# Kernel tuning notes

Hardware: AMD Instinct MI355X
Metric: run time of the kernel (lower is better)

Reference implementation:

```python
import jax, jax.numpy as jnp
import numpy as np
from jax import lax

MAX_C = 16       # MAX_MERGE_NUMS
COND_THRES = 0.2
IOU_THRES = 0.3
CLASS_OFFSET = 1e4  # shift per-class so cross-class BEV IoU == 0 (emulates per-class loop)


def setup_inputs() -> dict:
    key = jax.random.key(0)
    k1, k2, k3, k4, k5 = jax.random.split(key, 5)
    B, N = 4, 4096
    # realistic 3D boxes: centers, positive sizes, heading
    centers = jax.random.normal(k1, (B, N, 3), jnp.float32) * 20.0
    sizes = jax.random.uniform(k2, (B, N, 3), jnp.float32, 0.5, 4.5)
    heading = jax.random.uniform(k3, (B, N, 1), jnp.float32, -np.pi, np.pi)
    boxes = jnp.concatenate([centers, sizes, heading], -1)  # [B,N,7]
    scores = jax.random.uniform(k4, (B, N), jnp.float32)
    labels = jax.random.randint(k5, (B, N), 0, 3, jnp.int32)
    kw = jax.random.split(jax.random.fold_in(key, 1), 2)
    W1 = jax.random.normal(kw[0], (7, 64), jnp.float32) * 0.3
    b1 = jnp.zeros((64,), jnp.float32)
    W2 = jax.random.normal(kw[1], (64, 1), jnp.float32) * 0.3
    b2 = jnp.zeros((1,), jnp.float32)
    return {"boxes": boxes, "scores": scores, "labels": labels,
            "W1": W1, "b1": b1, "W2": W2, "b2": b2}


def _nms_merge_frame(boxes, scores, labels, W1, b1, W2, b2):
    # boxes [N,7], scores [N], labels [N] int32
    N = boxes.shape[0]
    valid = scores > COND_THRES                       # cond_mask
    skey = jnp.where(valid, scores, -jnp.inf)
    order = jnp.argsort(-skey)                        # score descending
    boxes, scores = boxes[order], scores[order]
    labels, valid = labels[order], valid[order]

    # nearest-BEV (axis-aligned) IoU; class offset keeps classes disjoint
    off = labels.astype(boxes.dtype) * CLASS_OFFSET
    cx, cy = boxes[:, 0] + off, boxes[:, 1]
    hx, hy = boxes[:, 3] * 0.5, boxes[:, 4] * 0.5
    x1, x2, y1, y2 = cx - hx, cx + hx, cy - hy, cy + hy
    ix = jnp.clip(jnp.minimum(x2[:, None], x2[None]) - jnp.maximum(x1[:, None], x1[None]), 0.0)
    iy = jnp.clip(jnp.minimum(y2[:, None], y2[None]) - jnp.maximum(y1[:, None], y1[None]), 0.0)
    inter = ix * iy                                   # [N,N]
    area = (x2 - x1) * (y2 - y1)
    iou = inter / jnp.clip(area[:, None] + area[None] - inter, 1e-6)
    overlap = iou > IOU_THRES                         # includes self

    # greedy clustering: highest-score remaining box leads its cluster
    def body(i, st):
        alive, cid = st
        lead = alive[i]
        take = alive & overlap[i] & lead
        cid = jnp.where(take, i, cid)
        return alive & (~take), cid
    alive, cid = lax.fori_loop(0, N, body,
                               (valid, jnp.full((N,), -1, jnp.int32)))
    leader = cid == jnp.arange(N, dtype=jnp.int32)    # cluster representatives

    # rank of each box within its cluster (score order preserved)
    idx = jnp.arange(N)
    same = (cid[None, :] == cid[:, None]) & (cid[:, None] >= 0)
    rank = (same & (idx[None, :] < idx[:, None])).sum(-1)  # [N]

    # scatter up to MAX_C members per cluster (zero-padded buffers)
    dest = jnp.where((cid >= 0) & (rank < MAX_C), cid, N)  # N = dump row
    clusters = jnp.zeros((N + 1, MAX_C, 7), boxes.dtype)
    clusters = clusters.at[dest, jnp.minimum(rank, MAX_C - 1)].set(boxes)[:N]

    # merge network: per-box MLP -> softmax weights over cluster slots
    h = jax.nn.relu(clusters @ W1 + b1)               # [N,MAX_C,64]
    logits = (h @ W2 + b2)[..., 0]                    # [N,MAX_C]
    slot_ok = jnp.any(clusters != 0, -1)
    logits = jnp.where(slot_ok, logits, -1e9)
    w = jax.nn.softmax(logits, -1)
    merged = jnp.einsum('nc,ncd->nd', w, clusters)    # [N,7]

    # masked scatter: non-positive merged sizes fall back to leader sizes
    size = jnp.where(merged[:, 3:6] <= 0, boxes[:, 3:6], merged[:, 3:6])
    out_box = jnp.concatenate([merged[:, :3], size, merged[:, 6:7]], -1)
    info = jnp.concatenate([out_box, scores[:, None],
                            labels.astype(boxes.dtype)[:, None]], -1)  # [N,9]
    info = jnp.where(leader[:, None], info, 0.0)
    return info, leader


def reference(boxes, scores, labels, W1, b1, W2, b2):
    info, leader = jax.vmap(_nms_merge_frame,
                            in_axes=(0, 0, 0, None, None, None, None))(
        boxes, scores, labels, W1, b1, W2, b2)
    return info, leader
```

## Files before the change

kernel.cpp:

```cpp
#include <hip/hip_runtime.h>
#include <stdint.h>

#pragma clang fp contract(off)

#define BF 4
#define NN 4096
#define MAXC 16
#define PL 2048
#define WL 32
#define WF 24
#define TRI_CAP (64 * (WL * (WL + 1) / 2))

typedef unsigned long long u64;
typedef uint32_t u32;

#define WAVE_SYNC() asm volatile("s_waitcnt lgkmcnt(0)" ::: "memory")

__device__ __forceinline__ u64 shfl64(u64 v, int src) {
  return (u64)__shfl((long long)v, src, 64);
}
__device__ __forceinline__ u64 readlane64(u64 v, int l) {
  u32 lo = (u32)__builtin_amdgcn_readlane((int)(u32)v, l);
  u32 hi = (u32)__builtin_amdgcn_readlane((int)(u32)(v >> 32), l);
  return ((u64)hi << 32) | lo;
}
__device__ __forceinline__ u64 greedy64_iso(u64 D, u64 rem, u64 onlyme) {
  u64 lead = 0;
  while (rem) {
    u64 t = D & rem;
    u64 iso = __ballot(t == onlyme) & rem;
    lead |= iso;
    rem &= ~iso;
    if (!rem) break;
    int b = __builtin_ctzll(rem);
    lead |= 1ull << b;
    rem &= ~readlane64(D, b);
    if (!rem) break;
    b = __builtin_ctzll(rem);
    lead |= 1ull << b;
    rem &= ~readlane64(D, b);
  }
  return lead;
}

__global__ __launch_bounds__(256) void rg_kernel(
    const float* __restrict__ scores, const float* __restrict__ boxes,
    const int* __restrict__ labels,
    float* __restrict__ sboxes, float* __restrict__ sscore, float* __restrict__ slabel,
    int* __restrict__ lab_slot, int* __restrict__ loc_slot,
    int* __restrict__ pglob,
    float* __restrict__ px1, float* __restrict__ px2, float* __restrict__ py1,
    float* __restrict__ py2, float* __restrict__ parea,
    int* __restrict__ VbufL)
{
  __shared__ u64 keys[NN];
  __shared__ int cnt[4][64];
  __shared__ int lcnt[4][64];
  __shared__ int vc[4][3];
  const int f = blockIdx.x >> 6, rb = blockIdx.x & 63;
  const int tid = threadIdx.x, wave = tid >> 6, lane = tid & 63;
  for (int s = 0; s < 16; s++) {
    int idx = tid + 256 * s;
    float sc = scores[f * NN + idx];
    bool valid = sc > 0.2f;
    int lab = labels[f * NN + idx];
    u32 bits = __float_as_uint(sc);
    u32 m = bits ^ ((bits >> 31) ? 0xFFFFFFFFu : 0x80000000u);
    u32 hi = valid ? ~m : 0xFFFFFFFFu;
    u32 lo = ((u32)idx << 2) | (valid ? (u32)lab : 3u);
    keys[idx] = ((u64)hi << 32) | lo;
  }
  __syncthreads();
  if (rb == 0) {
    int c0 = 0, c1 = 0, c2 = 0;
    const int base = wave * 1024;
    for (int s = 0; s < 16; s++) {
      u32 lb = (u32)keys[base + s * 64 + lane] & 3u;
      c0 += (lb == 0); c1 += (lb == 1); c2 += (lb == 2);
    }
    for (int off = 32; off; off >>= 1) {
      c0 += __shfl_xor(c0, off, 64);
      c1 += __shfl_xor(c1, off, 64);
      c2 += __shfl_xor(c2, off, 64);
    }
    if (lane == 0) { vc[wave][0] = c0; vc[wave][1] = c1; vc[wave][2] = c2; }
  }
  const int row = rb * 64 + lane;
  const u64 mykey = keys[row];
  const u32 mylab = (u32)mykey & 3u;
  int c = 0, lc = 0;
  const int j0 = wave * 1024;
#pragma unroll 8
  for (int j = j0; j < j0 + 1024; j++) {
    u64 kj = keys[j];
    bool lt = kj < mykey;
    c += lt ? 1 : 0;
    lc += (lt && (((u32)kj & 3u) == mylab)) ? 1 : 0;
  }
  cnt[wave][lane] = c;
  lcnt[wave][lane] = lc;
  __syncthreads();
  if (rb == 0 && wave == 1 && lane < 3)
    VbufL[f * 3 + lane] = vc[0][lane] + vc[1][lane] + vc[2][lane] + vc[3][lane];
  if (wave == 0) {
    int rank = cnt[0][lane] + cnt[1][lane] + cnt[2][lane] + cnt[3][lane];
    int loc  = lcnt[0][lane] + lcnt[1][lane] + lcnt[2][lane] + lcnt[3][lane];
    const int i = row;
    const float* bp = boxes + (size_t)(f * NN + i) * 7;
    float b0 = bp[0], b1v = bp[1], b2v = bp[2], b3 = bp[3], b4 = bp[4], b5 = bp[5], b6 = bp[6];
    int lab = labels[f * NN + i];
    float sc = scores[f * NN + i];
    const int o = f * NN + rank;
    float* sb = sboxes + (size_t)o * 7;
    sb[0] = b0; sb[1] = b1v; sb[2] = b2v; sb[3] = b3; sb[4] = b4; sb[5] = b5; sb[6] = b6;
    sscore[o] = sc;
    slabel[o] = (float)lab;
    if (mylab < 3u) {
      int pi = (f * 3 + (int)mylab) * PL + loc;
      float off = (float)mylab * 10000.0f;
      float cx = b0 + off, cy = b1v;
      float hx = b3 * 0.5f, hy = b4 * 0.5f;
      float x1 = cx - hx, x2 = cx + hx, y1 = cy - hy, y2 = cy + hy;
      float area = (x2 - x1) * (y2 - y1);
      pglob[pi] = rank;
      px1[pi] = x1; px2[pi] = x2; py1[pi] = y1; py2[pi] = y2; parea[pi] = area;
      lab_slot[o] = (int)mylab; loc_slot[o] = loc;
    } else {
      lab_slot[o] = -1; loc_slot[o] = -1;
    }
  }
}

__global__ __launch_bounds__(256) void mask_kernel(
    const float* __restrict__ px1, const float* __restrict__ px2,
    const float* __restrict__ py1, const float* __restrict__ py2,
    const float* __restrict__ parea, const int* __restrict__ pglob,
    const int* __restrict__ VbufL,
    u64* __restrict__ maskP, u64* __restrict__ triT)
{
  __shared__ float4 cbox[1024];
  __shared__ float carea[1024];
  const int bx = blockIdx.x;
  const int fl = bx >> 8, rem = bx & 255;
  const int rt = rem >> 1, wt = rem & 1;
  const int r0 = rt * 16;
  const int Vl = VbufL[fl];
  if (r0 >= Vl) return;
  if (wt * 1024 >= Vl) return;
  const int tid = threadIdx.x;
  const int ncol = Vl - wt * 1024;
  const int nload = (ncol < 1024) ? ncol : 1024;
  for (int q = tid; q < nload; q += 256) {
    int c = fl * PL + wt * 1024 + q;
    cbox[q] = make_float4(px1[c], px2[c], py1[c], py2[c]);
    carea[q] = parea[c];
  }
  __syncthreads();
  const int row = r0 + (tid & 15);
  const int wl = tid >> 4;
  const int cw = wt * 16 + wl;
  const int nc = Vl - cw * 64;
  if (row >= Vl || nc <= 0) return;
  const int rg = fl * PL + row;
  const float rx1 = px1[rg], rx2 = px2[rg], ry1 = py1[rg], ry2 = py2[rg], ra = parea[rg];
  u64 bits = 0;
  const int qb = wl * 64;
  for (int b = 0; b < 64; b++) {
    float4 cb = cbox[qb + b];
    float ca = carea[qb + b];
    float ix = fminf(rx2, cb.y) - fmaxf(rx1, cb.x);
    ix = fmaxf(ix, 0.0f);
    float iy = fminf(ry2, cb.w) - fmaxf(ry1, cb.z);
    iy = fmaxf(iy, 0.0f);
    float inter = ix * iy;
    float den = fmaxf((ra + ca) - inter, 1e-6f);
    float iou = inter / den;
    bits |= ((u64)(iou > 0.3f)) << b;
  }
  if (nc < 64) bits &= (1ull << nc) - 1ull;
  const int f = fl / 3;
  const int p = pglob[fl * PL + row];
  maskP[((size_t)f * NN + p) * WL + cw] = bits;
  if (row >= 64 * cw) {
    const int W = (Vl + 63) >> 6;
    int base = 64 * (cw * W - (cw * (cw - 1)) / 2);
    triT[(size_t)fl * TRI_CAP + base + (row - 64 * cw)] = bits;
  }
}

__global__ __launch_bounds__(64) void nms_kernel(
    const u64* __restrict__ triT, const int* __restrict__ VbufL,
    u64* __restrict__ leadersP)
{
  __shared__ u64 tri[64 * (WF * (WF + 1) / 2) + 128];
  const int fl = blockIdx.x, lane = threadIdx.x;
  const int Vl = VbufL[fl];
  const int W = (Vl + 63) >> 6;
  const u64* mT = triT + (size_t)fl * TRI_CAP;
  const u64 onlyme = 1ull << lane;
  u64 alive = 0;
  if (lane < WL) {
    int rb = Vl - 64 * lane;
    alive = (rb >= 64) ? ~0ull : ((rb > 0) ? ((1ull << rb) - 1ull) : 0ull);
  }
  u64 myLead = 0;

  if (W > 0 && W <= WF) {
    const int totw = 64 * (W * (W + 1) / 2);
    const int nch = (totw * 8 + 1023) >> 10;
    const char* g = (const char*)mT;
    char* l = (char*)tri;
    int batch = 0;
    for (int it = 0; it < nch; it++) {
      __builtin_amdgcn_global_load_lds(
          (const __attribute__((address_space(1))) unsigned int*)(g + (size_t)it * 1024 + (size_t)lane * 16),
          (__attribute__((address_space(3))) unsigned int*)(l + (size_t)it * 1024),
          16, 0, 0);
      if (++batch == 48) {
        asm volatile("s_waitcnt vmcnt(0)" ::: "memory");
        batch = 0;
      }
    }
    asm volatile("s_waitcnt vmcnt(0)" ::: "memory");
    int offw = 0;
    u64 D = tri[lane];
    for (int w = 0; w < W; w++) {
      const int offw_next = offw + 64 * (W - w);
      u64 Dnext = (w + 1 < W) ? tri[offw_next + lane] : 0;
      u64 lead = greedy64_iso(D, readlane64(alive, w), onlyme);
      if (lane == w) myLead = lead;
      if (lead) {
        const u64* strm = tri + offw;
        int v = w + 1;
        for (; v + 3 < W; v += 4) {
          u64 a0 = strm[64 * (v - w) + lane];
          u64 a1 = strm[64 * (v + 1 - w) + lane];
          u64 a2 = strm[64 * (v + 2 - w) + lane];
          u64 a3 = strm[64 * (v + 3 - w) + lane];
          u64 c0 = __ballot((a0 & lead) != 0ull);
          u64 c1 = __ballot((a1 & lead) != 0ull);
          u64 c2 = __ballot((a2 & lead) != 0ull);
          u64 c3 = __ballot((a3 & lead) != 0ull);
          if (lane == v)     alive &= ~c0;
          if (lane == v + 1) alive &= ~c1;
          if (lane == v + 2) alive &= ~c2;
          if (lane == v + 3) alive &= ~c3;
        }
        for (; v < W; v++) {
          u64 a0 = strm[64 * (v - w) + lane];
          u64 c0 = __ballot((a0 & lead) != 0ull);
          if (lane == v) alive &= ~c0;
        }
      }
      D = Dnext;
      offw = offw_next;
    }
  } else if (W > 0) {
    int offw = 0;
    for (int w = 0; w < W; w++) {
      const u64* strm = mT + offw;
      u64 D = strm[lane];
      u64 lead = greedy64_iso(D, readlane64(alive, w), onlyme);
      if (lane == w) myLead = lead;
      if (lead) {
        for (int v = w + 1; v < W; v++) {
          u64 a0 = strm[64 * (v - w) + lane];
          u64 c0 = __ballot((a0 & lead) != 0ull);
          if (lane == v) alive &= ~c0;
        }
      }
      offw += 64 * (W - w);
    }
  }
  if (lane < WL) leadersP[fl * WL + lane] = myLead;
}

__global__ __launch_bounds__(256) void cid_kernel(
    const u64* __restrict__ maskP, const u64* __restrict__ leadersP,
    const int* __restrict__ lab_slot, const int* __restrict__ loc_slot,
    const int* __restrict__ VbufL, int* __restrict__ cidP)
{
  const int g = blockIdx.x * 4 + (threadIdx.x >> 6);
  const int lane = threadIdx.x & 63;
  const int f = g >> 12, p = g & (NN - 1);
  const int l = lab_slot[f * NN + p];
  if (l < 0) return;
  const int fl = f * 3 + l;
  const int loc = loc_slot[f * NN + p];
  const int Wl = (VbufL[fl] + 63) >> 6;
  u64 L = 0, m = 0;
  if (lane < Wl) {
    L = leadersP[fl * WL + lane];
    m = maskP[((size_t)f * NN + p) * WL + lane];
  }
  const int g6 = loc >> 6, b6 = loc & 63;
  u64 pmask = (lane < g6) ? ~0ull
            : (lane == g6 ? ((b6 == 63) ? ~0ull : ((1ull << (b6 + 1)) - 1ull)) : 0ull);
  u64 v = m & L & pmask;
  u64 bl = __ballot(v != 0ull);
  int cid = -1;
  if (bl != 0ull) {
    int w = __builtin_ctzll(bl);
    u64 vw = shfl64(v, w);
    cid = w * 64 + __builtin_ctzll(vw);
  }
  if (lane == 0) cidP[fl * PL + loc] = cid;
}

__global__ __launch_bounds__(256) void mm_kernel(
    const u64* __restrict__ maskP, const u64* __restrict__ leadersP,
    const int* __restrict__ cidP, const int* __restrict__ lab_slot,
    const int* __restrict__ loc_slot, const int* __restrict__ pglob,
    const int* __restrict__ VbufL,
    const float* __restrict__ sboxes, const float* __restrict__ sscore,
    const float* __restrict__ slabel,
    const float* __restrict__ W1, const float* __restrict__ b1,
    const float* __restrict__ W2, const float* __restrict__ b2,
    float* __restrict__ out)
{
  __shared__ int   mlistS[4][MAXC];
  __shared__ float mbS[4][MAXC][7];
  __shared__ float lgS[4][MAXC];
  __shared__ float wnS[4][MAXC];
  const int wv = threadIdx.x >> 6, lane = threadIdx.x & 63;
  const int bi = blockIdx.x * 4 + wv;
  const int f = bi >> 12, i = bi & (NN - 1);
  const int o = f * NN + i;
  float* info = out + (size_t)o * 9;
  float* lead = out + (size_t)BF * NN * 9 + o;
  const int l = lab_slot[o];
  bool isLead = false;
  int loc = 0, fl = 0;
  if (l >= 0) {
    fl = f * 3 + l;
    loc = loc_slot[o];
    isLead = (leadersP[fl * WL + (loc >> 6)] >> (loc & 63)) & 1ull;
  }
  if (!isLead) {
    if (lane < 9) info[lane] = 0.0f;
    if (lane == 0) *lead = 0.0f;
    return;
  }
  int* mlist = mlistS[wv];
  float (*mb)[7] = mbS[wv];
  float* lg = lgS[wv];
  float* wn = wnS[wv];
  const u64* mrow = maskP + (size_t)o * WL;
  const int Wl = (VbufL[fl] + 63) >> 6;
  int total = 0;
  for (int w = loc >> 6; w < Wl && total < MAXC; w++) {
    u64 word = mrow[w];
    int pos = w * 64 + lane;
    bool cand = ((word >> lane) & 1ull) && (cidP[fl * PL + pos] == loc);
    u64 mbal = __ballot(cand);
    int r = __popcll(mbal & ((1ull << lane) - 1ull));
    int slot = total + r;
    if (cand && slot < MAXC) mlist[slot] = pglob[fl * PL + pos];
    total += __popcll(mbal);
  }
  const int cnt = min(total, MAXC);
  WAVE_SYNC();
  if (lane < cnt) {
    int j = mlist[lane];
    const float* bp = sboxes + (size_t)(f * NN + j) * 7;
    for (int d = 0; d < 7; d++) mb[lane][d] = bp[d];
  }
  float w1r[7];
  for (int d = 0; d < 7; d++) w1r[d] = W1[d * 64 + lane];
  const float b1c = b1[lane], w2c = W2[lane], b2v = b2[0];
  WAVE_SYNC();
  for (int s = 0; s < cnt; s++) {
    float t = b1c;
    for (int d = 0; d < 7; d++) t += mb[s][d] * w1r[d];
    float h = fmaxf(t, 0.0f);
    float v = h * w2c;
    for (int off2 = 32; off2 > 0; off2 >>= 1) v += __shfl_xor(v, off2, 64);
    if (lane == 0) lg[s] = v + b2v;
  }
  WAVE_SYNC();
  float mx = -1e30f;
  for (int s = 0; s < cnt; s++) mx = fmaxf(mx, lg[s]);
  float den = 0.0f;
  for (int s = 0; s < cnt; s++) den += expf(lg[s] - mx);
  if (lane < cnt) wn[lane] = expf(lg[lane] - mx) / den;
  WAVE_SYNC();
  float val = 0.0f;
  if (lane < 7) {
    float acc = 0.0f;
    for (int s = 0; s < cnt; s++) acc += wn[s] * mb[s][lane];
    val = acc;
    if (lane >= 3 && lane <= 5 && val <= 0.0f) val = sboxes[(size_t)o * 7 + lane];
  } else if (lane == 7) {
    val = sscore[o];
  } else if (lane == 8) {
    val = slabel[o];
  }
  if (lane < 9) info[lane] = val;
  if (lane == 0) *lead = 1.0f;
}

extern "C" void kernel_launch(void* const* d_in, const int* in_sizes, int n_in,
                              void* d_out, int out_size, void* d_ws, size_t ws_size,
                              hipStream_t stream)
{
  const float* boxes  = (const float*)d_in[0];
  const float* scores = (const float*)d_in[1];
  const int*   labels = (const int*)d_in[2];
  const float* W1     = (const float*)d_in[3];
  const float* b1     = (const float*)d_in[4];
  const float* W2     = (const float*)d_in[5];
  const float* b2     = (const float*)d_in[6];
  float* out = (float*)d_out;

  char* ws = (char*)d_ws;
  size_t off = 0;
  auto alloc = [&](size_t bytes) -> void* {
    void* p = ws + off;
    off = (off + bytes + 255) & ~(size_t)255;
    return p;
  };
  float* sboxes  = (float*)alloc((size_t)BF * NN * 7 * 4);
  float* sscore  = (float*)alloc((size_t)BF * NN * 4);
  float* slabel  = (float*)alloc((size_t)BF * NN * 4);
  int*   lab_slot= (int*)  alloc((size_t)BF * NN * 4);
  int*   loc_slot= (int*)  alloc((size_t)BF * NN * 4);
  int*   pglob   = (int*)  alloc((size_t)BF * 3 * PL * 4);
  float* px1     = (float*)alloc((size_t)BF * 3 * PL * 4);
  float* px2     = (float*)alloc((size_t)BF * 3 * PL * 4);
  float* py1     = (float*)alloc((size_t)BF * 3 * PL * 4);
  float* py2     = (float*)alloc((size_t)BF * 3 * PL * 4);
  float* parea   = (float*)alloc((size_t)BF * 3 * PL * 4);
  int*   VbufL   = (int*)  alloc((size_t)BF * 3 * 4);
  u64*   leadersP= (u64*)  alloc((size_t)BF * 3 * WL * 8);
  int*   cidP    = (int*)  alloc((size_t)BF * 3 * PL * 4);
  u64*   maskP   = (u64*)  alloc((size_t)BF * NN * WL * 8);
  u64*   triT    = (u64*)  alloc((size_t)BF * 3 * TRI_CAP * 8);
  (void)  alloc(32768);

  rg_kernel<<<BF * 64, 256, 0, stream>>>(scores, boxes, labels, sboxes,
                                         sscore, slabel, lab_slot, loc_slot,
                                         pglob, px1, px2, py1, py2, parea,
                                         VbufL);
  mask_kernel<<<BF * 3 * 256, 256, 0, stream>>>(px1, px2, py1, py2, parea,
                                                pglob, VbufL, maskP, triT);
  nms_kernel<<<BF * 3, 64, 0, stream>>>(triT, VbufL, leadersP);
  cid_kernel<<<BF * NN / 4, 256, 0, stream>>>(maskP, leadersP, lab_slot,
                                              loc_slot, VbufL, cidP);
  mm_kernel<<<BF * NN / 4, 256, 0, stream>>>(maskP, leadersP, cidP, lab_slot,
                                             loc_slot, pglob, VbufL, sboxes,
                                             sscore, slabel, W1, b1, W2, b2, out);
}
```

Baseline: 156.8 us.

## Fuse five pipeline kernels into one persistent kernel with grid barriers

Replaces the five separate launches (rank/gather, IoU mask, NMS, cluster-id, merge) with a single persistent kernel of 256 blocks. Stages are separated by atomic-counter grid barriers, and a memset resets the counters before each launch. The aim is to remove per-launch overhead and inter-kernel gaps. In exchange, the mask, cid and merge stages run with a fixed 256-block grid in grid-stride loops, and NMS still runs on only 12 single-wave blocks while the rest of the grid waits at a barrier. The spin barriers rely on all blocks being co-resident and have a timeout escape.

New measurement: 438.6 us. 180% more time.

```diff
diff --git a/kernel.cpp b/kernel.cpp
--- a/kernel.cpp
+++ b/kernel.cpp
@@ -42,376 +42,378 @@
   }
   return lead;
 }
-
-__global__ __launch_bounds__(256) void rg_kernel(
-    const float* __restrict__ scores, const float* __restrict__ boxes,
-    const int* __restrict__ labels,
-    float* __restrict__ sboxes, float* __restrict__ sscore, float* __restrict__ slabel,
-    int* __restrict__ lab_slot, int* __restrict__ loc_slot,
-    int* __restrict__ pglob,
-    float* __restrict__ px1, float* __restrict__ px2, float* __restrict__ py1,
-    float* __restrict__ py2, float* __restrict__ parea,
-    int* __restrict__ VbufL)
+__device__ __forceinline__ int loadVl(const int* VbufL, int fl) {
+  int v = VbufL[fl];
+  return (v < 0) ? 0 : ((v > PL) ? PL : v);
+}
+
+__device__ __forceinline__ void gbar(int* bar, int k) {
+  __syncthreads();
+  __threadfence();
+  if (threadIdx.x == 0) {
+    atomicAdd(&bar[k], 1);
+    long long t0 = clock64();
+    while (__hip_atomic_load(&bar[k], __ATOMIC_RELAXED,
+                             __HIP_MEMORY_SCOPE_AGENT) < (int)gridDim.x) {
+      __builtin_amdgcn_s_sleep(2);
+      if (clock64() - t0 > (3LL << 30)) break;
+    }
+  }
+  __syncthreads();
+  __threadfence();
+}
+
+struct Prm {
+  const float* scores; const float* boxes; const int* labels;
+  const float* W1; const float* b1; const float* W2; const float* b2;
+  float* sboxes; float* sscore; float* slabel;
+  int* lab_slot; int* loc_slot; int* pglob;
+  float* px1; float* px2; float* py1; float* py2; float* parea;
+  int* VbufL; u64* leadersP; int* cidP; u64* maskP; u64* triT;
+  int* bar;
+  float* out;
+};
+
+__global__ __launch_bounds__(256, 1) void fused_kernel(Prm pr)
 {
-  __shared__ u64 keys[NN];
-  __shared__ int cnt[4][64];
-  __shared__ int lcnt[4][64];
-  __shared__ int vc[4][3];
-  const int f = blockIdx.x >> 6, rb = blockIdx.x & 63;
+  __shared__ u64 SM[19500];
   const int tid = threadIdx.x, wave = tid >> 6, lane = tid & 63;
-  for (int s = 0; s < 16; s++) {
-    int idx = tid + 256 * s;
-    float sc = scores[f * NN + idx];
-    bool valid = sc > 0.2f;
-    int lab = labels[f * NN + idx];
-    u32 bits = __float_as_uint(sc);
-    u32 m = bits ^ ((bits >> 31) ? 0xFFFFFFFFu : 0x80000000u);
-    u32 hi = valid ? ~m : 0xFFFFFFFFu;
-    u32 lo = ((u32)idx << 2) | (valid ? (u32)lab : 3u);
-    keys[idx] = ((u64)hi << 32) | lo;
-  }
-  __syncthreads();
-  if (rb == 0) {
-    int c0 = 0, c1 = 0, c2 = 0;
-    const int base = wave * 1024;
+  const u64 ltmask = (1ull << lane) - 1ull;
+
+  {
+    u64* keys = SM;
+    int* cnt  = (int*)&SM[4096];
+    int* lcnt = (int*)&SM[4224];
+    int* vc   = (int*)&SM[4352];
+    const int f = blockIdx.x >> 6, rb = blockIdx.x & 63;
     for (int s = 0; s < 16; s++) {
-      u32 lb = (u32)keys[base + s * 64 + lane] & 3u;
-      c0 += (lb == 0); c1 += (lb == 1); c2 += (lb == 2);
-    }
-    for (int off = 32; off; off >>= 1) {
-      c0 += __shfl_xor(c0, off, 64);
-      c1 += __shfl_xor(c1, off, 64);
-      c2 += __shfl_xor(c2, off, 64);
-    }
-    if (lane == 0) { vc[wave][0] = c0; vc[wave][1] = c1; vc[wave][2] = c2; }
-  }
-  const int row = rb * 64 + lane;
-  const u64 mykey = keys[row];
-  const u32 mylab = (u32)mykey & 3u;
-  int c = 0, lc = 0;
-  const int j0 = wave * 1024;
+      int idx = tid + 256 * s;
+      float sc = pr.scores[f * NN + idx];
+      bool valid = sc > 0.2f;
+      int lab = pr.labels[f * NN + idx];
+      u32 bits = __float_as_uint(sc);
+      u32 m = bits ^ ((bits >> 31) ? 0xFFFFFFFFu : 0x80000000u);
+      u32 hi = valid ? ~m : 0xFFFFFFFFu;
+      u32 lo = ((u32)idx << 2) | (valid ? (u32)lab : 3u);
+      keys[idx] = ((u64)hi << 32) | lo;
+    }
+    __syncthreads();
+    if (rb == 0) {
+      int c0 = 0, c1 = 0, c2 = 0;
+      const int base = wave * 1024;
+      for (int s = 0; s < 16; s++) {
+        u32 lb = (u32)keys[base + s * 64 + lane] & 3u;
+        c0 += (lb == 0); c1 += (lb == 1); c2 += (lb == 2);
+      }
+      for (int off = 32; off; off >>= 1) {
+        c0 += __shfl_xor(c0, off, 64);
+        c1 += __shfl_xor(c1, off, 64);
+        c2 += __shfl_xor(c2, off, 64);
+      }
+      if (lane == 0) { vc[wave * 3 + 0] = c0; vc[wave * 3 + 1] = c1; vc[wave * 3 + 2] = c2; }
+    }
+    const int row = rb * 64 + lane;
+    const u64 mykey = keys[row];
+    const u32 mylab = (u32)mykey & 3u;
+    int c = 0, lc = 0;
+    const int j0 = wave * 1024;
 #pragma unroll 8
-  for (int j = j0; j < j0 + 1024; j++) {
-    u64 kj = keys[j];
-    bool lt = kj < mykey;
-    c += lt ? 1 : 0;
-    lc += (lt && (((u32)kj & 3u) == mylab)) ? 1 : 0;
-  }
-  cnt[wave][lane] = c;
-  lcnt[wave][lane] = lc;
-  __syncthreads();
-  if (rb == 0 && wave == 1 && lane < 3)
-    VbufL[f * 3 + lane] = vc[0][lane] + vc[1][lane] + vc[2][lane] + vc[3][lane];
-  if (wave == 0) {
-    int rank = cnt[0][lane] + cnt[1][lane] + cnt[2][lane] + cnt[3][lane];
-    int loc  = lcnt[0][lane] + lcnt[1][lane] + lcnt[2][lane] + lcnt[3][lane];
-    const int i = row;
-    const float* bp = boxes + (size_t)(f * NN + i) * 7;
-    float b0 = bp[0], b1v = bp[1], b2v = bp[2], b3 = bp[3], b4 = bp[4], b5 = bp[5], b6 = bp[6];
-    int lab = labels[f * NN + i];
-    float sc = scores[f * NN + i];
-    const int o = f * NN + rank;
-    float* sb = sboxes + (size_t)o * 7;
-    sb[0] = b0; sb[1] = b1v; sb[2] = b2v; sb[3] = b3; sb[4] = b4; sb[5] = b5; sb[6] = b6;
-    sscore[o] = sc;
-    slabel[o] = (float)lab;
-    if (mylab < 3u) {
-      int pi = (f * 3 + (int)mylab) * PL + loc;
-      float off = (float)mylab * 10000.0f;
-      float cx = b0 + off, cy = b1v;
-      float hx = b3 * 0.5f, hy = b4 * 0.5f;
-      float x1 = cx - hx, x2 = cx + hx, y1 = cy - hy, y2 = cy + hy;
-      float area = (x2 - x1) * (y2 - y1);
-      pglob[pi] = rank;
-      px1[pi] = x1; px2[pi] = x2; py1[pi] = y1; py2[pi] = y2; parea[pi] = area;
-      lab_slot[o] = (int)mylab; loc_slot[o] = loc;
-    } else {
-      lab_slot[o] = -1; loc_slot[o] = -1;
-    }
-  }
-}
-
-__global__ __launch_bounds__(256) void mask_kernel(
-    const float* __restrict__ px1, const float* __restrict__ px2,
-    const float* __restrict__ py1, const float* __restrict__ py2,
-    const float* __restrict__ parea, const int* __restrict__ pglob,
-    const int* __restrict__ VbufL,
-    u64* __restrict__ maskP, u64* __restrict__ triT)
-{
-  __shared__ float4 cbox[1024];
-  __shared__ float carea[1024];
-  const int bx = blockIdx.x;
-  const int fl = bx >> 8, rem = bx & 255;
-  const int rt = rem >> 1, wt = rem & 1;
-  const int r0 = rt * 16;
-  const int Vl = VbufL[fl];
-  if (r0 >= Vl) return;
-  if (wt * 1024 >= Vl) return;
-  const int tid = threadIdx.x;
-  const int ncol = Vl - wt * 1024;
-  const int nload = (ncol < 1024) ? ncol : 1024;
-  for (int q = tid; q < nload; q += 256) {
-    int c = fl * PL + wt * 1024 + q;
-    cbox[q] = make_float4(px1[c], px2[c], py1[c], py2[c]);
-    carea[q] = parea[c];
-  }
-  __syncthreads();
-  const int row = r0 + (tid & 15);
-  const int wl = tid >> 4;
-  const int cw = wt * 16 + wl;
-  const int nc = Vl - cw * 64;
-  if (row >= Vl || nc <= 0) return;
-  const int rg = fl * PL + row;
-  const float rx1 = px1[rg], rx2 = px2[rg], ry1 = py1[rg], ry2 = py2[rg], ra = parea[rg];
-  u64 bits = 0;
-  const int qb = wl * 64;
-  for (int b = 0; b < 64; b++) {
-    float4 cb = cbox[qb + b];
-    float ca = carea[qb + b];
-    float ix = fminf(rx2, cb.y) - fmaxf(rx1, cb.x);
-    ix = fmaxf(ix, 0.0f);
-    float iy = fminf(ry2, cb.w) - fmaxf(ry1, cb.z);
-    iy = fmaxf(iy, 0.0f);
-    float inter = ix * iy;
-    float den = fmaxf((ra + ca) - inter, 1e-6f);
-    float iou = inter / den;
-    bits |= ((u64)(iou > 0.3f)) << b;
-  }
-  if (nc < 64) bits &= (1ull << nc) - 1ull;
-  const int f = fl / 3;
-  const int p = pglob[fl * PL + row];
-  maskP[((size_t)f * NN + p) * WL + cw] = bits;
-  if (row >= 64 * cw) {
+    for (int j = j0; j < j0 + 1024; j++) {
+      u64 kj = keys[j];
+      bool lt = kj < mykey;
+      c += lt ? 1 : 0;
+      lc += (lt && (((u32)kj & 3u) == mylab)) ? 1 : 0;
+    }
+    cnt[wave * 64 + lane] = c;
+    lcnt[wave * 64 + lane] = lc;
+    __syncthreads();
+    if (rb == 0 && wave == 1 && lane < 3)
+      pr.VbufL[f * 3 + lane] = vc[0 * 3 + lane] + vc[1 * 3 + lane]
+                             + vc[2 * 3 + lane] + vc[3 * 3 + lane];
+    if (wave == 0) {
+      int rank = cnt[lane] + cnt[64 + lane] + cnt[128 + lane] + cnt[192 + lane];
+      int loc  = lcnt[lane] + lcnt[64 + lane] + lcnt[128 + lane] + lcnt[192 + lane];
+      const int i = row;
+      const float* bp = pr.boxes + (size_t)(f * NN + i) * 7;
+      float b0 = bp[0], b1v = bp[1], b2v = bp[2], b3 = bp[3], b4 = bp[4], b5 = bp[5], b6 = bp[6];
+      int lab = pr.labels[f * NN + i];
+      float sc = pr.scores[f * NN + i];
+      const int o = f * NN + rank;
+      float* sb = pr.sboxes + (size_t)o * 7;
+      sb[0] = b0; sb[1] = b1v; sb[2] = b2v; sb[3] = b3; sb[4] = b4; sb[5] = b5; sb[6] = b6;
+      pr.sscore[o] = sc;
+      pr.slabel[o] = (float)lab;
+      if (mylab < 3u) {
+        int pi = (f * 3 + (int)mylab) * PL + loc;
+        float off = (float)mylab * 10000.0f;
+        float cx = b0 + off, cy = b1v;
+        float hx = b3 * 0.5f, hy = b4 * 0.5f;
+        float x1 = cx - hx, x2 = cx + hx, y1 = cy - hy, y2 = cy + hy;
+        float area = (x2 - x1) * (y2 - y1);
+        pr.pglob[pi] = rank;
+        pr.px1[pi] = x1; pr.px2[pi] = x2; pr.py1[pi] = y1; pr.py2[pi] = y2;
+        pr.parea[pi] = area;
+        pr.lab_slot[o] = (int)mylab; pr.loc_slot[o] = loc;
+      } else {
+        pr.lab_slot[o] = -1; pr.loc_slot[o] = -1;
+      }
+    }
+  }
+  gbar(pr.bar, 0);
+
+  {
+    float4* cbox = (float4*)SM;
+    float*  carea = (float*)&SM[2048];
+    for (int vt = blockIdx.x; vt < BF * 3 * 256; vt += 256) {
+      __syncthreads();
+      const int fl = vt >> 8, rem = vt & 255;
+      const int rt = rem >> 1, wt = rem & 1;
+      const int r0 = rt * 16;
+      const int Vl = loadVl(pr.VbufL, fl);
+      const bool act = (r0 < Vl) && (wt * 1024 < Vl);
+      if (act) {
+        const int ncol = Vl - wt * 1024;
+        const int nload = (ncol < 1024) ? ncol : 1024;
+        for (int q = tid; q < nload; q += 256) {
+          int cc = fl * PL + wt * 1024 + q;
+          cbox[q] = make_float4(pr.px1[cc], pr.px2[cc], pr.py1[cc], pr.py2[cc]);
+          carea[q] = pr.parea[cc];
+        }
+      }
+      __syncthreads();
+      if (!act) continue;
+      const int row = r0 + (tid & 15);
+      const int wl = tid >> 4;
+      const int cw = wt * 16 + wl;
+      const int nc = Vl - cw * 64;
+      if (row < Vl && nc > 0) {
+        const int rg = fl * PL + row;
+        const float rx1 = pr.px1[rg], rx2 = pr.px2[rg];
+        const float ry1 = pr.py1[rg], ry2 = pr.py2[rg], ra = pr.parea[rg];
+        u64 bits = 0;
+        const int qb = wl * 64;
+        for (int b = 0; b < 64; b++) {
+          float4 cb = cbox[qb + b];
+          float ca = carea[qb + b];
+          float ix = fminf(rx2, cb.y) - fmaxf(rx1, cb.x);
+          ix = fmaxf(ix, 0.0f);
+          float iy = fminf(ry2, cb.w) - fmaxf(ry1, cb.z);
+          iy = fmaxf(iy, 0.0f);
+          float inter = ix * iy;
+          float den = fmaxf((ra + ca) - inter, 1e-6f);
+          float iou = inter / den;
+          bits |= ((u64)(iou > 0.3f)) << b;
+        }
+        if (nc < 64) bits &= (1ull << nc) - 1ull;
+        const int f = fl / 3;
+        const int p = pr.pglob[fl * PL + row] & (NN - 1);
+        pr.maskP[((size_t)f * NN + p) * WL + cw] = bits;
+        if (row >= 64 * cw) {
+          const int W = (Vl + 63) >> 6;
+          int base = 64 * (cw * W - (cw * (cw - 1)) / 2);
+          pr.triT[(size_t)fl * TRI_CAP + base + (row - 64 * cw)] = bits;
+        }
+      }
+    }
+  }
+  gbar(pr.bar, 1);
+
+  if (blockIdx.x < BF * 3 && wave == 0) {
+    u64* tri = SM;
+    const int fl = blockIdx.x;
+    const int Vl = loadVl(pr.VbufL, fl);
     const int W = (Vl + 63) >> 6;
-    int base = 64 * (cw * W - (cw * (cw - 1)) / 2);
-    triT[(size_t)fl * TRI_CAP + base + (row - 64 * cw)] = bits;
-  }
-}
-
-__global__ __launch_bounds__(64) void nms_kernel(
-    const u64* __restrict__ triT, const int* __restrict__ VbufL,
-    u64* __restrict__ leadersP)
-{
-  __shared__ u64 tri[64 * (WF * (WF + 1) / 2) + 128];
-  const int fl = blockIdx.x, lane = threadIdx.x;
-  const int Vl = VbufL[fl];
-  const int W = (Vl + 63) >> 6;
-  const u64* mT = triT + (size_t)fl * TRI_CAP;
-  const u64 onlyme = 1ull << lane;
-  u64 alive = 0;
-  if (lane < WL) {
-    int rb = Vl - 64 * lane;
-    alive = (rb >= 64) ? ~0ull : ((rb > 0) ? ((1ull << rb) - 1ull) : 0ull);
-  }
-  u64 myLead = 0;
-
-  if (W > 0 && W <= WF) {
-    const int totw = 64 * (W * (W + 1) / 2);
-    const int nch = (totw * 8 + 1023) >> 10;
-    const char* g = (const char*)mT;
-    char* l = (char*)tri;
-    int batch = 0;
-    for (int it = 0; it < nch; it++) {
-      __builtin_amdgcn_global_load_lds(
-          (const __attribute__((address_space(1))) unsigned int*)(g + (size_t)it * 1024 + (size_t)lane * 16),
-          (__attribute__((address_space(3))) unsigned int*)(l + (size_t)it * 1024),
-          16, 0, 0);
-      if (++batch == 48) {
-        asm volatile("s_waitcnt vmcnt(0)" ::: "memory");
-        batch = 0;
-      }
-    }
-    asm volatile("s_waitcnt vmcnt(0)" ::: "memory");
-    int offw = 0;
-    u64 D = tri[lane];
-    for (int w = 0; w < W; w++) {
-      const int offw_next = offw + 64 * (W - w);
-      u64 Dnext = (w + 1 < W) ? tri[offw_next + lane] : 0;
-      u64 lead = greedy64_iso(D, readlane64(alive, w), onlyme);
-      if (lane == w) myLead = lead;
-      if (lead) {
-        const u64* strm = tri + offw;
-        int v = w + 1;
-        for (; v + 3 < W; v += 4) {
-          u64 a0 = strm[64 * (v - w) + lane];
-          u64 a1 = strm[64 * (v + 1 - w) + lane];
-          u64 a2 = strm[64 * (v + 2 - w) + lane];
-          u64 a3 = strm[64 * (v + 3 - w) + lane];
-          u64 c0 = __ballot((a0 & lead) != 0ull);
-          u64 c1 = __ballot((a1 & lead) != 0ull);
-          u64 c2 = __ballot((a2 & lead) != 0ull);
-          u64 c3 = __ballot((a3 & lead) != 0ull);
-          if (lane == v)     alive &= ~c0;
-          if (lane == v + 1) alive &= ~c1;
-          if (lane == v + 2) alive &= ~c2;
-          if (lane == v + 3) alive &= ~c3;
-        }
-        for (; v < W; v++) {
-          u64 a0 = strm[64 * (v - w) + lane];
-          u64 c0 = __ballot((a0 & lead) != 0ull);
-          if (lane == v) alive &= ~c0;
-        }
-      }
-      D = Dnext;
-      offw = offw_next;
-    }
-  } else if (W > 0) {
-    int offw = 0;
-    for (int w = 0; w < W; w++) {
-      const u64* strm = mT + offw;
-      u64 D = strm[lane];
-      u64 lead = greedy64_iso(D, readlane64(alive, w), onlyme);
-      if (lane == w) myLead = lead;
-      if (lead) {
-        for (int v = w + 1; v < W; v++) {
-          u64 a0 = strm[64 * (v - w) + lane];
-          u64 c0 = __ballot((a0 & lead) != 0ull);
-          if (lane == v) alive &= ~c0;
-        }
-      }
-      offw += 64 * (W - w);
-    }
-  }
-  if (lane < WL) leadersP[fl * WL + lane] = myLead;
-}
-
-__global__ __launch_bounds__(256) void cid_kernel(
-    const u64* __restrict__ maskP, const u64* __restrict__ leadersP,
-    const int* __restrict__ lab_slot, const int* __restrict__ loc_slot,
-    const int* __restrict__ VbufL, int* __restrict__ cidP)
-{
-  const int g = blockIdx.x * 4 + (threadIdx.x >> 6);
-  const int lane = threadIdx.x & 63;
-  const int f = g >> 12, p = g & (NN - 1);
-  const int l = lab_slot[f * NN + p];
-  if (l < 0) return;
-  const int fl = f * 3 + l;
-  const int loc = loc_slot[f * NN + p];
-  const int Wl = (VbufL[fl] + 63) >> 6;
-  u64 L = 0, m = 0;
-  if (lane < Wl) {
-    L = leadersP[fl * WL + lane];
-    m = maskP[((size_t)f * NN + p) * WL + lane];
-  }
-  const int g6 = loc >> 6, b6 = loc & 63;
-  u64 pmask = (lane < g6) ? ~0ull
-            : (lane == g6 ? ((b6 == 63) ? ~0ull : ((1ull << (b6 + 1)) - 1ull)) : 0ull);
-  u64 v = m & L & pmask;
-  u64 bl = __ballot(v != 0ull);
-  int cid = -1;
-  if (bl != 0ull) {
-    int w = __builtin_ctzll(bl);
-    u64 vw = shfl64(v, w);
-    cid = w * 64 + __builtin_ctzll(vw);
-  }
-  if (lane == 0) cidP[fl * PL + loc] = cid;
-}
-
-__global__ __launch_bounds__(256) void mm_kernel(
-    const u64* __restrict__ maskP, const u64* __restrict__ leadersP,
-    const int* __restrict__ cidP, const int* __restrict__ lab_slot,
-    const int* __restrict__ loc_slot, const int* __restrict__ pglob,
-    const int* __restrict__ VbufL,
-    const float* __restrict__ sboxes, const float* __restrict__ sscore,
-    const float* __restrict__ slabel,
-    const float* __restrict__ W1, const float* __restrict__ b1,
-    const float* __restrict__ W2, const float* __restrict__ b2,
-    float* __restrict__ out)
-{
-  __shared__ int   mlistS[4][MAXC];
-  __shared__ float mbS[4][MAXC][7];
-  __shared__ float lgS[4][MAXC];
-  __shared__ float wnS[4][MAXC];
-  const int wv = threadIdx.x >> 6, lane = threadIdx.x & 63;
-  const int bi = blockIdx.x * 4 + wv;
-  const int f = bi >> 12, i = bi & (NN - 1);
-  const int o = f * NN + i;
-  float* info = out + (size_t)o * 9;
-  float* lead = out + (size_t)BF * NN * 9 + o;
-  const int l = lab_slot[o];
-  bool isLead = false;
-  int loc = 0, fl = 0;
-  if (l >= 0) {
-    fl = f * 3 + l;
-    loc = loc_slot[o];
-    isLead = (leadersP[fl * WL + (loc >> 6)] >> (loc & 63)) & 1ull;
-  }
-  if (!isLead) {
-    if (lane < 9) info[lane] = 0.0f;
-    if (lane == 0) *lead = 0.0f;
-    return;
-  }
-  int* mlist = mlistS[wv];
-  float (*mb)[7] = mbS[wv];
-  float* lg = lgS[wv];
-  float* wn = wnS[wv];
-  const u64* mrow = maskP + (size_t)o * WL;
-  const int Wl = (VbufL[fl] + 63) >> 6;
-  int total = 0;
-  for (int w = loc >> 6; w < Wl && total < MAXC; w++) {
-    u64 word = mrow[w];
-    int pos = w * 64 + lane;
-    bool cand = ((word >> lane) & 1ull) && (cidP[fl * PL + pos] == loc);
-    u64 mbal = __ballot(cand);
-    int r = __popcll(mbal & ((1ull << lane) - 1ull));
-    int slot = total + r;
-    if (cand && slot < MAXC) mlist[slot] = pglob[fl * PL + pos];
-    total += __popcll(mbal);
-  }
-  const int cnt = min(total, MAXC);
-  WAVE_SYNC();
-  if (lane < cnt) {
-    int j = mlist[lane];
-    const float* bp = sboxes + (size_t)(f * NN + j) * 7;
-    for (int d = 0; d < 7; d++) mb[lane][d] = bp[d];
-  }
-  float w1r[7];
-  for (int d = 0; d < 7; d++) w1r[d] = W1[d * 64 + lane];
-  const float b1c = b1[lane], w2c = W2[lane], b2v = b2[0];
-  WAVE_SYNC();
-  for (int s = 0; s < cnt; s++) {
-    float t = b1c;
-    for (int d = 0; d < 7; d++) t += mb[s][d] * w1r[d];
-    float h = fmaxf(t, 0.0f);
-    float v = h * w2c;
-    for (int off2 = 32; off2 > 0; off2 >>= 1) v += __shfl_xor(v, off2, 64);
-    if (lane == 0) lg[s] = v + b2v;
-  }
-  WAVE_SYNC();
-  float mx = -1e30f;
-  for (int s = 0; s < cnt; s++) mx = fmaxf(mx, lg[s]);
-  float den = 0.0f;
-  for (int s = 0; s < cnt; s++) den += expf(lg[s] - mx);
-  if (lane < cnt) wn[lane] = expf(lg[lane] - mx) / den;
-  WAVE_SYNC();
-  float val = 0.0f;
-  if (lane < 7) {
-    float acc = 0.0f;
-    for (int s = 0; s < cnt; s++) acc += wn[s] * mb[s][lane];
-    val = acc;
-    if (lane >= 3 && lane <= 5 && val <= 0.0f) val = sboxes[(size_t)o * 7 + lane];
-  } else if (lane == 7) {
-    val = sscore[o];
-  } else if (lane == 8) {
-    val = slabel[o];
-  }
-  if (lane < 9) info[lane] = val;
-  if (lane == 0) *lead = 1.0f;
+    const u64* mT = pr.triT + (size_t)fl * TRI_CAP;
+    const u64 onlyme = 1ull << lane;
+    u64 alive = 0;
+    if (lane < WL) {
+      int rb2 = Vl - 64 * lane;
+      alive = (rb2 >= 64) ? ~0ull : ((rb2 > 0) ? ((1ull << rb2) - 1ull) : 0ull);
+    }
+    u64 myLead = 0;
+    if (W > 0 && W <= WF) {
+      const int totw = 64 * (W * (W + 1) / 2);
+      const int nch = (totw * 8 + 1023) >> 10;
+      const char* g = (const char*)mT;
+      char* l = (char*)tri;
+      int batch = 0;
+      for (int it = 0; it < nch; it++) {
+        __builtin_amdgcn_global_load_lds(
+            (const __attribute__((address_space(1))) unsigned int*)(g + (size_t)it * 1024 + (size_t)lane * 16),
+            (__attribute__((address_space(3))) unsigned int*)(l + (size_t)it * 1024),
+            16, 0, 0);
+        if (++batch == 48) {
+          asm volatile("s_waitcnt vmcnt(0)" ::: "memory");
+          batch = 0;
+        }
+      }
+      asm volatile("s_waitcnt vmcnt(0)" ::: "memory");
+      int offw = 0;
+      u64 D = tri[lane];
+      for (int w = 0; w < W; w++) {
+        const int offw_next = offw + 64 * (W - w);
+        u64 Dnext = (w + 1 < W) ? tri[offw_next + lane] : 0;
+        u64 lead = greedy64_iso(D, readlane64(alive, w), onlyme);
+        if (lane == w) myLead = lead;
+        if (lead) {
+          const u64* strm = tri + offw;
+          int v = w + 1;
+          for (; v + 3 < W; v += 4) {
+            u64 a0 = strm[64 * (v - w) + lane];
+            u64 a1 = strm[64 * (v + 1 - w) + lane];
+            u64 a2 = strm[64 * (v + 2 - w) + lane];
+            u64 a3 = strm[64 * (v + 3 - w) + lane];
+            u64 c0 = __ballot((a0 & lead) != 0ull);
+            u64 c1 = __ballot((a1 & lead) != 0ull);
+            u64 c2 = __ballot((a2 & lead) != 0ull);
+            u64 c3 = __ballot((a3 & lead) != 0ull);
+            if (lane == v)     alive &= ~c0;
+            if (lane == v + 1) alive &= ~c1;
+            if (lane == v + 2) alive &= ~c2;
+            if (lane == v + 3) alive &= ~c3;
+          }
+          for (; v < W; v++) {
+            u64 a0 = strm[64 * (v - w) + lane];
+            u64 c0 = __ballot((a0 & lead) != 0ull);
+            if (lane == v) alive &= ~c0;
+          }
+        }
+        D = Dnext;
+        offw = offw_next;
+      }
+    } else if (W > 0) {
+      int offw = 0;
+      for (int w = 0; w < W; w++) {
+        const u64* strm = mT + offw;
+        u64 D = strm[lane];
+        u64 lead = greedy64_iso(D, readlane64(alive, w), onlyme);
+        if (lane == w) myLead = lead;
+        if (lead) {
+          for (int v = w + 1; v < W; v++) {
+            u64 a0 = strm[64 * (v - w) + lane];
+            u64 c0 = __ballot((a0 & lead) != 0ull);
+            if (lane == v) alive &= ~c0;
+          }
+        }
+        offw += 64 * (W - w);
+      }
+    }
+    if (lane < WL) pr.leadersP[fl * WL + lane] = myLead;
+  }
+  gbar(pr.bar, 2);
+
+  for (int g = blockIdx.x * 4 + wave; g < BF * NN; g += 1024) {
+    const int f = g >> 12, p = g & (NN - 1);
+    const int l = pr.lab_slot[f * NN + p];
+    if (l < 0) continue;
+    const int fl = f * 3 + l;
+    const int loc = pr.loc_slot[f * NN + p];
+    const int Wl = (loadVl(pr.VbufL, fl) + 63) >> 6;
+    u64 L = 0, m = 0;
+    if (lane < Wl) {
+      L = pr.leadersP[fl * WL + lane];
+      m = pr.maskP[((size_t)f * NN + p) * WL + lane];
+    }
+    const int g6 = loc >> 6, b6 = loc & 63;
+    u64 pmask = (lane < g6) ? ~0ull
+              : (lane == g6 ? ((b6 == 63) ? ~0ull : ((1ull << (b6 + 1)) - 1ull)) : 0ull);
+    u64 v = m & L & pmask;
+    u64 bl = __ballot(v != 0ull);
+    int cid = -1;
+    if (bl != 0ull) {
+      int w = __builtin_ctzll(bl);
+      u64 vw = shfl64(v, w);
+      cid = w * 64 + __builtin_ctzll(vw);
+    }
+    if (lane == 0) pr.cidP[fl * PL + loc] = cid;
+  }
+  gbar(pr.bar, 3);
+
+  {
+    u64* base = &SM[wave * 80];
+    int*   mlist = (int*)base;
+    float* mbv   = (float*)(base + 8);
+    float* lg    = (float*)(base + 64);
+    float* wn    = (float*)(base + 72);
+    float w1r[7];
+    for (int d = 0; d < 7; d++) w1r[d] = pr.W1[d * 64 + lane];
+    const float b1c = pr.b1[lane], w2c = pr.W2[lane], b2v = pr.b2[0];
+    for (int g = blockIdx.x * 4 + wave; g < BF * NN; g += 1024) {
+      const int f = g >> 12, i = g & (NN - 1);
+      const int o = f * NN + i;
+      float* info = pr.out + (size_t)o * 9;
+      float* lead = pr.out + (size_t)BF * NN * 9 + o;
+      const int l = pr.lab_slot[o];
+      bool isLead = false;
+      int loc = 0, fl = 0;
+      if (l >= 0) {
+        fl = f * 3 + l;
+        loc = pr.loc_slot[o];
+        isLead = (pr.leadersP[fl * WL + (loc >> 6)] >> (loc & 63)) & 1ull;
+      }
+      if (!isLead) {
+        if (lane < 9) info[lane] = 0.0f;
+        if (lane == 0) *lead = 0.0f;
+        continue;
+      }
+      const u64* mrow = pr.maskP + (size_t)o * WL;
+      const int Wl = (loadVl(pr.VbufL, fl) + 63) >> 6;
+      int total = 0;
+      for (int w = loc >> 6; w < Wl && total < MAXC; w++) {
+        u64 word = mrow[w];
+        int pos = w * 64 + lane;
+        bool cand = ((word >> lane) & 1ull) && (pr.cidP[fl * PL + pos] == loc);
+        u64 mbal = __ballot(cand);
+        int r = __popcll(mbal & ltmask);
+        int slot = total + r;
+        if (cand && slot < MAXC) mlist[slot] = pr.pglob[fl * PL + pos];
+        total += __popcll(mbal);
+      }
+      const int cnt = min(total, MAXC);
+      WAVE_SYNC();
+      if (lane < cnt) {
+        int j = mlist[lane] & (NN - 1);
+        const float* bp = pr.sboxes + (size_t)(f * NN + j) * 7;
+        for (int d = 0; d < 7; d++) mbv[lane * 7 + d] = bp[d];
+      }
+      WAVE_SYNC();
+      for (int s = 0; s < cnt; s++) {
+        float t = b1c;
+        for (int d = 0; d < 7; d++) t += mbv[s * 7 + d] * w1r[d];
+        float h = fmaxf(t, 0.0f);
+        float v = h * w2c;
+        for (int off2 = 32; off2 > 0; off2 >>= 1) v += __shfl_xor(v, off2, 64);
+        if (lane == 0) lg[s] = v + b2v;
+      }
+      WAVE_SYNC();
+      float mx = -1e30f;
+      for (int s = 0; s < cnt; s++) mx = fmaxf(mx, lg[s]);
+      float den = 0.0f;
+      for (int s = 0; s < cnt; s++) den += expf(lg[s] - mx);
+      if (lane < cnt) wn[lane] = expf(lg[lane] - mx) / den;
+      WAVE_SYNC();
+      float val = 0.0f;
+      if (lane < 7) {
+        float acc = 0.0f;
+        for (int s = 0; s < cnt; s++) acc += wn[s] * mbv[s * 7 + lane];
+        val = acc;
+        if (lane >= 3 && lane <= 5 && val <= 0.0f) val = pr.sboxes[(size_t)o * 7 + lane];
+      } else if (lane == 7) {
+        val = pr.sscore[o];
+      } else if (lane == 8) {
+        val = pr.slabel[o];
+      }
+      if (lane < 9) info[lane] = val;
+      if (lane == 0) *lead = 1.0f;
+      WAVE_SYNC();
+    }
+  }
 }
 
 extern "C" void kernel_launch(void* const* d_in, const int* in_sizes, int n_in,
                               void* d_out, int out_size, void* d_ws, size_t ws_size,
                               hipStream_t stream)
 {
-  const float* boxes  = (const float*)d_in[0];
-  const float* scores = (const float*)d_in[1];
-  const int*   labels = (const int*)d_in[2];
-  const float* W1     = (const float*)d_in[3];
-  const float* b1     = (const float*)d_in[4];
-  const float* W2     = (const float*)d_in[5];
-  const float* b2     = (const float*)d_in[6];
-  float* out = (float*)d_out;
-
   char* ws = (char*)d_ws;
   size_t off = 0;
   auto alloc = [&](size_t bytes) -> void* {
@@ -419,34 +421,34 @@
     off = (off + bytes + 255) & ~(size_t)255;
     return p;
   };
-  float* sboxes  = (float*)alloc((size_t)BF * NN * 7 * 4);
-  float* sscore  = (float*)alloc((size_t)BF * NN * 4);
-  float* slabel  = (float*)alloc((size_t)BF * NN * 4);
-  int*   lab_slot= (int*)  alloc((size_t)BF * NN * 4);
-  int*   loc_slot= (int*)  alloc((size_t)BF * NN * 4);
-  int*   pglob   = (int*)  alloc((size_t)BF * 3 * PL * 4);
-  float* px1     = (float*)alloc((size_t)BF * 3 * PL * 4);
-  float* px2     = (float*)alloc((size_t)BF * 3 * PL * 4);
-  float* py1     = (float*)alloc((size_t)BF * 3 * PL * 4);
-  float* py2     = (float*)alloc((size_t)BF * 3 * PL * 4);
-  float* parea   = (float*)alloc((size_t)BF * 3 * PL * 4);
-  int*   VbufL   = (int*)  alloc((size_t)BF * 3 * 4);
-  u64*   leadersP= (u64*)  alloc((size_t)BF * 3 * WL * 8);
-  int*   cidP    = (int*)  alloc((size_t)BF * 3 * PL * 4);
-  u64*   maskP   = (u64*)  alloc((size_t)BF * NN * WL * 8);
-  u64*   triT    = (u64*)  alloc((size_t)BF * 3 * TRI_CAP * 8);
-  (void)  alloc(32768);
-
-  rg_kernel<<<BF * 64, 256, 0, stream>>>(scores, boxes, labels, sboxes,
-                                         sscore, slabel, lab_slot, loc_slot,
-                                         pglob, px1, px2, py1, py2, parea,
-                                         VbufL);
-  mask_kernel<<<BF * 3 * 256, 256, 0, stream>>>(px1, px2, py1, py2, parea,
-                                                pglob, VbufL, maskP, triT);
-  nms_kernel<<<BF * 3, 64, 0, stream>>>(triT, VbufL, leadersP);
-  cid_kernel<<<BF * NN / 4, 256, 0, stream>>>(maskP, leadersP, lab_slot,
-                                              loc_slot, VbufL, cidP);
-  mm_kernel<<<BF * NN / 4, 256, 0, stream>>>(maskP, leadersP, cidP, lab_slot,
-                                             loc_slot, pglob, VbufL, sboxes,
-                                             sscore, slabel, W1, b1, W2, b2, out);
-}
+  Prm pr;
+  pr.scores = (const float*)d_in[1];
+  pr.boxes  = (const float*)d_in[0];
+  pr.labels = (const int*)d_in[2];
+  pr.W1 = (const float*)d_in[3];
+  pr.b1 = (const float*)d_in[4];
+  pr.W2 = (const float*)d_in[5];
+  pr.b2 = (const float*)d_in[6];
+  pr.out = (float*)d_out;
+  pr.bar     = (int*)  alloc(256);
+  pr.sboxes  = (float*)alloc((size_t)BF * NN * 7 * 4);
+  pr.sscore  = (float*)alloc((size_t)BF * NN * 4);
+  pr.slabel  = (float*)alloc((size_t)BF * NN * 4);
+  pr.lab_slot= (int*)  alloc((size_t)BF * NN * 4);
+  pr.loc_slot= (int*)  alloc((size_t)BF * NN * 4);
+  pr.pglob   = (int*)  alloc((size_t)BF * 3 * PL * 4);
+  pr.px1     = (float*)alloc((size_t)BF * 3 * PL * 4);
+  pr.px2     = (float*)alloc((size_t)BF * 3 * PL * 4);
+  pr.py1     = (float*)alloc((size_t)BF * 3 * PL * 4);
+  pr.py2     = (float*)alloc((size_t)BF * 3 * PL * 4);
+  pr.parea   = (float*)alloc((size_t)BF * 3 * PL * 4);
+  pr.VbufL   = (int*)  alloc((size_t)BF * 3 * 4);
+  pr.leadersP= (u64*)  alloc((size_t)BF * 3 * WL * 8);
+  pr.cidP    = (int*)  alloc((size_t)BF * 3 * PL * 4);
+  pr.maskP   = (u64*)  alloc((size_t)BF * NN * WL * 8);
+  pr.triT    = (u64*)  alloc((size_t)BF * 3 * TRI_CAP * 8);
+  (void)      alloc(32768);
+
+  hipMemsetAsync(pr.bar, 0, 256, stream);
+  fused_kernel<<<dim3(256), dim3(256), 0, stream>>>(pr);
+}
```
